# Kernel tuning notes

Measured on AMD Instinct MI355X. Metric: run time of the kernel, lower is better.

## Reference

```python
import jax, jax.numpy as jnp
import numpy as np

N = 8192          # number of prototypes
D = 128           # proto_dim == hidden_dim (residual requires equality)
H = 2             # GAT heads
K = 3             # k_neighbors + 1 (k_neighbors=2 hard-coded in forward)
NEG_SLOPE = 0.2   # PyG GATConv default leaky relu slope
LN_EPS = 1e-5


def setup_inputs() -> dict:
    key = jax.random.key(0)
    ks = jax.random.split(key, 6)
    prototypes = jax.random.normal(ks[0], (N, D), dtype=jnp.float32)
    labels = jax.random.randint(ks[1], (N,), 0, 1024, dtype=jnp.int64)
    # GATConv params: lin maps D -> H*D (concat=False => per-head dim = hidden_dim)
    W = jax.random.normal(ks[2], (D, H * D), dtype=jnp.float32) / np.sqrt(D)
    att_src = jax.random.normal(ks[3], (H, D), dtype=jnp.float32) / np.sqrt(D)
    att_dst = jax.random.normal(ks[4], (H, D), dtype=jnp.float32) / np.sqrt(D)
    bias = jnp.zeros((D,), dtype=jnp.float32)
    gamma = jnp.ones((D,), dtype=jnp.float32)   # LayerNorm weight
    beta = jnp.zeros((D,), dtype=jnp.float32)   # LayerNorm bias
    return {"prototypes": prototypes, "labels": labels, "W": W,
            "att_src": att_src, "att_dst": att_dst, "bias": bias,
            "gamma": gamma, "beta": beta}


def _knn_edges(x):
    # Squared euclidean distances (same ordering as torch.cdist -> same topk indices).
    sq = jnp.sum(x * x, axis=-1)
    d2 = sq[:, None] + sq[None, :] - 2.0 * (x @ x.T)          # [N, N]
    _, idx = jax.lax.top_k(-d2, K)                            # [N, K] smallest dists
    # topk includes self (dist 0); module masks self-edges then GATConv re-adds
    # self loops, so the effective edge set is exactly the topk set -> static E=N*K.
    src = jnp.repeat(jnp.arange(x.shape[0]), K)               # edge source j
    dst = idx.reshape(-1)                                     # edge target i
    return src, dst


def _gat(x, src, dst, W, att_src, att_dst, bias):
    n = x.shape[0]
    xp = (x @ W).reshape(n, H, D)                             # [N, H, C]
    a_s = jnp.sum(xp * att_src[None], axis=-1)                # [N, H]
    a_d = jnp.sum(xp * att_dst[None], axis=-1)                # [N, H]
    e = a_s[src] + a_d[dst]                                   # [E, H]
    e = jax.nn.leaky_relu(e, NEG_SLOPE)
    # segment softmax over incoming edges of each destination node
    m = jax.ops.segment_max(e, dst, num_segments=n)           # [N, H]
    w = jnp.exp(e - m[dst])
    denom = jax.ops.segment_sum(w, dst, num_segments=n)       # [N, H]
    alpha = w / denom[dst]                                    # [E, H]
    msg = alpha[:, :, None] * xp[src]                         # [E, H, C]
    out = jax.ops.segment_sum(msg, dst, num_segments=n)       # [N, H, C]
    return out.mean(axis=1) + bias                            # concat=False -> head mean


def reference(prototypes, labels, W, att_src, att_dst, bias, gamma, beta):
    x = prototypes
    src, dst = _knn_edges(x)
    x_new = _gat(x, src, dst, W, att_src, att_dst, bias)
    mu = jnp.mean(x_new, axis=-1, keepdims=True)
    var = jnp.var(x_new, axis=-1, keepdims=True)
    x_new = (x_new - mu) * jax.lax.rsqrt(var + LN_EPS) * gamma + beta
    x_new = jax.nn.relu(x_new)
    # dropout layers are identity in eval mode
    return x + x_new
```

## Files before the change

### kernel.cpp

```cpp
#include <hip/hip_runtime.h>
#include <hip/hip_bf16.h>
#include <math.h>

#define GN 8192
#define GD 128
#define GH 2
#define GK 3
#define NEG_SLOPE 0.2f
#define LN_EPS 1e-5f

using short8  = __attribute__((ext_vector_type(8)))  short;
using float16 = __attribute__((ext_vector_type(16))) float;
using f32x4   = __attribute__((ext_vector_type(4)))  float;

__device__ __forceinline__ float wred(float v) {
    #pragma unroll
    for (int o = 32; o > 0; o >>= 1) v += __shfl_xor(v, o, 64);
    return v;
}

__device__ __forceinline__ unsigned fenc(float f) {
    unsigned b = __float_as_uint(f);
    return (b & 0x80000000u) ? ~b : (b | 0x80000000u);
}

__device__ __forceinline__ float rawbf2f(unsigned short s) {
    return __uint_as_float(((unsigned)s) << 16);
}
__device__ __forceinline__ unsigned short f2rawbf(float f) {
    __hip_bfloat16 b = __float2bfloat16(f);
    unsigned short r; __builtin_memcpy(&r, &b, 2);
    return r;
}
__device__ __forceinline__ unsigned umin2(unsigned a, unsigned b) { return a < b ? a : b; }
__device__ __forceinline__ unsigned umax2(unsigned a, unsigned b) { return a > b ? a : b; }

__global__ void k_zero(int* p, int n) {
    int t = blockIdx.x * 256 + threadIdx.x;
    if (t < n) p[t] = 0;
}

__global__ void k_uvec(const float* __restrict__ W, const float* __restrict__ att_src,
                       const float* __restrict__ att_dst, float* __restrict__ uvec) {
    __shared__ float vs[128];
    int b = blockIdx.x, t = threadIdx.x;
    int h = b & 1;
    const float* v = (b < 2 ? att_src : att_dst) + h * 128;
    if (t < 128) vs[t] = v[t];
    __syncthreads();
    int d = t >> 1, half = t & 1;
    const float* wr = W + (size_t)d * 256 + h * 128 + half * 64;
    float s = 0.f;
    for (int c = 0; c < 64; c++) s += wr[c] * vs[half * 64 + c];
    s += __shfl_xor(s, 1, 64);
    if (half == 0) uvec[b * 128 + d] = s;
}

__global__ void k_trans(const float* __restrict__ W,
                        unsigned short* __restrict__ Wth, unsigned short* __restrict__ Wtl) {
    int e = blockIdx.x * 256 + threadIdx.x;
    int d = e >> 8, j = e & 255;
    int h = j >> 7, c = j & 127;
    int k = h * 128 + d;
    float w = W[e];
    unsigned short hi = f2rawbf(w);
    Wth[c * 256 + k] = hi;
    Wtl[c * 256 + k] = f2rawbf(w - rawbf2f(hi));
}

__global__ void k_conv(const float* __restrict__ x, const float* __restrict__ uvec,
                       float* __restrict__ sq,
                       unsigned short* __restrict__ xa, unsigned short* __restrict__ xb,
                       float* __restrict__ a_s, float* __restrict__ a_d) {
    int row = blockIdx.x * 4 + (threadIdx.x >> 6);
    int lane = threadIdx.x & 63;
    const float* xr = x + (size_t)row * GD;
    float a0 = xr[lane], a1 = xr[lane + 64];
    float s = wred(a0 * a0 + a1 * a1);
    unsigned short* ar = xa + (size_t)row * 144;
    unsigned short* br = xb + (size_t)row * 144;
    ar[lane] = f2rawbf(-2.f * a0); ar[lane + 64] = f2rawbf(-2.f * a1);
    br[lane] = f2rawbf(a0);        br[lane + 64] = f2rawbf(a1);
    float s0 = wred(a0 * uvec[lane]       + a1 * uvec[64 + lane]);
    float s1 = wred(a0 * uvec[128 + lane] + a1 * uvec[192 + lane]);
    float d0 = wred(a0 * uvec[256 + lane] + a1 * uvec[320 + lane]);
    float d1 = wred(a0 * uvec[384 + lane] + a1 * uvec[448 + lane]);
    if (lane < 16) {
        unsigned short av = 0, bv = 0;
        if (lane == 0)      { av = f2rawbf(s + 512.f); bv = 0x3F80; }
        else if (lane == 1) { float hi = rawbf2f(f2rawbf(s + 512.f));
                              av = f2rawbf(s + 512.f - hi); bv = 0x3F80; }
        ar[128 + lane] = av; br[128 + lane] = bv;
        if (lane == 0) {
            sq[row] = s;
            a_s[row * 2] = s0; a_s[row * 2 + 1] = s1;
            a_d[row * 2] = d0; a_d[row * 2 + 1] = d1;
        }
    }
}

struct Top6 {
    unsigned a0, a1, a2, a3, a4, a5;
    __device__ __forceinline__ void init() { a0=a1=a2=a3=a4=a5=0xFFFFFFFFu; }
    __device__ __forceinline__ void insert(unsigned k) {
        unsigned m0 = umax2(a0, k);  a0 = umin2(a0, k);
        unsigned m1 = umax2(a1, m0); a1 = umin2(a1, m0);
        unsigned m2 = umax2(a2, m1); a2 = umin2(a2, m1);
        unsigned m3 = umax2(a3, m2); a3 = umin2(a3, m2);
        unsigned m4 = umax2(a4, m3); a4 = umin2(a4, m3);
        a5 = umin2(a5, m4);
    }
};

__launch_bounds__(256, 2)
__global__ void k_gemm_topk(const unsigned short* __restrict__ xa,
                            const unsigned short* __restrict__ xb,
                            unsigned* __restrict__ cand) {
    __shared__ unsigned short At[18 * 128 * 8];
    int t = threadIdx.x;
    int w = t >> 6, lane = t & 63, h = lane >> 5, n = lane & 31;
    int col = blockIdx.x * 128 + w * 32 + n;
    int sb = blockIdx.y;

    short8 bfrag[9];
    #pragma unroll
    for (int kc = 0; kc < 9; kc++)
        bfrag[kc] = *(const short8*)(xb + (size_t)col * 144 + (2 * kc + h) * 8);

    Top6 T; T.init();

    for (int it = 0; it < 8; it++) {
        int rowbase = sb * 1024 + it * 128;
        __syncthreads();
        #pragma unroll
        for (int q = t; q < 18 * 128; q += 256) {
            int kb = q >> 7, r = q & 127;
            *(uint4*)&At[(kb * 128 + r) * 8] =
                *(const uint4*)(xa + (size_t)(rowbase + r) * 144 + kb * 8);
        }
        __syncthreads();

        float16 acc[4];
        #pragma unroll
        for (int rs = 0; rs < 4; rs++) acc[rs] = (float16)(0.f);

        #pragma unroll
        for (int kc = 0; kc < 9; kc++) {
            short8 a[4];
            #pragma unroll
            for (int rs = 0; rs < 4; rs++)
                a[rs] = *(const short8*)&At[((2 * kc + h) * 128 + rs * 32 + n) * 8];
            #pragma unroll
            for (int rs = 0; rs < 4; rs++)
                acc[rs] = __builtin_amdgcn_mfma_f32_32x32x16_bf16(a[rs], bfrag[kc], acc[rs], 0, 0, 0);
        }

        #pragma unroll
        for (int rs = 0; rs < 4; rs++) {
            float16 A = acc[rs];
            int rb = rowbase + 4 * h + rs * 32;
            unsigned kk[16];
            #pragma unroll
            for (int r = 0; r < 16; r++)
                kk[r] = (__float_as_uint(A[r]) & 0xFFFFE000u) |
                        (unsigned)(rb + (r & 3) + 8 * (r >> 2));
            unsigned ma = umin2(umin2(umin2(kk[0],kk[1]),umin2(kk[2],kk[3])),
                                umin2(umin2(kk[4],kk[5]),umin2(kk[6],kk[7])));
            unsigned mb = umin2(umin2(umin2(kk[8],kk[9]),umin2(kk[10],kk[11])),
                                umin2(umin2(kk[12],kk[13]),umin2(kk[14],kk[15])));
            if (umin2(ma, mb) <= T.a5) {
                #pragma unroll
                for (int r = 0; r < 16; r++) T.insert(kk[r]);
            }
        }
    }

    unsigned p0 = (unsigned)__shfl_xor((int)T.a0, 32), p1 = (unsigned)__shfl_xor((int)T.a1, 32),
             p2 = (unsigned)__shfl_xor((int)T.a2, 32), p3 = (unsigned)__shfl_xor((int)T.a3, 32),
             p4 = (unsigned)__shfl_xor((int)T.a4, 32), p5 = (unsigned)__shfl_xor((int)T.a5, 32);
    T.insert(p0); T.insert(p1); T.insert(p2); T.insert(p3); T.insert(p4); T.insert(p5);

    if (h == 0) {
        unsigned* c0 = cand + (size_t)col * 48 + sb * 6;
        c0[0]=T.a0; c0[1]=T.a1; c0[2]=T.a2; c0[3]=T.a3; c0[4]=T.a4; c0[5]=T.a5;
    }
}

__device__ __forceinline__ int clampN(int v) {
    return v < 0 ? 0 : (v >= GN ? GN - 1 : v);
}

__global__ void k_refine(const unsigned* __restrict__ cand,
                         const float* __restrict__ x, const float* __restrict__ sq,
                         int* __restrict__ fidx, int* __restrict__ cnt) {
    __shared__ float xjs[4][132];
    int t = threadIdx.x, wv = t >> 6, lane = t & 63;
    int j = blockIdx.x * 4 + wv;
    xjs[wv][lane] = x[(size_t)j * GD + lane];
    xjs[wv][64 + lane] = x[(size_t)j * GD + 64 + lane];
    float sqj = sq[j];
    unsigned long long key = ~0ull;
    if (lane < 48) {
        int idx = (int)(cand[(size_t)j * 48 + lane] & 8191u);
        const float* xi = x + (size_t)idx * GD;
        float p = 0.f;
        #pragma unroll
        for (int d4 = 0; d4 < 32; d4++) {
            float4 a = *(const float4*)(xi + d4 * 4);
            float4 b = *(const float4*)&xjs[wv][d4 * 4];
            p += a.x * b.x + a.y * b.y + a.z * b.z + a.w * b.w;
        }
        float d2 = sqj + sq[idx] - 2.f * p;
        key = ((unsigned long long)fenc(d2) << 32) | (unsigned)idx;
    }
    int out3[3];
    #pragma unroll
    for (int r = 0; r < 3; r++) {
        unsigned long long k = key;
        #pragma unroll
        for (int o = 32; o > 0; o >>= 1) {
            unsigned long long other = __shfl_xor(k, o, 64);
            k = k < other ? k : other;
        }
        out3[r] = (int)(unsigned)(k & 0xffffffffu);
        key = (key == k) ? ~0ull : key;
    }
    if (lane == 0) {
        int i0 = clampN(out3[0]), i1 = clampN(out3[1]), i2 = clampN(out3[2]);
        fidx[j * 3 + 0] = i0; fidx[j * 3 + 1] = i1; fidx[j * 3 + 2] = i2;
        atomicAdd(&cnt[i0], 1); atomicAdd(&cnt[i1], 1); atomicAdd(&cnt[i2], 1);
    }
}

__global__ void k_scan(const int* __restrict__ cnt, int* __restrict__ offs) {
    __shared__ int part[256];
    int t = threadIdx.x;
    int base = t * 32;
    int loc[32];
    int s = 0;
    #pragma unroll
    for (int k = 0; k < 32; k++) { loc[k] = s; s += cnt[base + k]; }
    part[t] = s;
    __syncthreads();
    if (t == 0) {
        int run = 0;
        for (int k = 0; k < 256; k++) { int v = part[k]; part[k] = run; run += v; }
        offs[GN] = run;
    }
    __syncthreads();
    int b = part[t];
    #pragma unroll
    for (int k = 0; k < 32; k++) offs[base + k] = b + loc[k];
}

__global__ void k_fill(const int* __restrict__ fidx, const int* __restrict__ offs,
                       int* __restrict__ cursor, int* __restrict__ elist,
                       const float* __restrict__ a_s, const float* __restrict__ a_d,
                       float2* __restrict__ ew) {
    int eid = blockIdx.x * 256 + threadIdx.x;
    int i = clampN(fidx[eid]);
    int src = eid / 3;
    float2 as = ((const float2*)a_s)[src];
    float2 ad = ((const float2*)a_d)[i];
    float e0 = as.x + ad.x; e0 = e0 >= 0.f ? e0 : NEG_SLOPE * e0;
    float e1 = as.y + ad.y; e1 = e1 >= 0.f ? e1 : NEG_SLOPE * e1;
    float w0 = expf(e0), w1 = expf(e1);
    int pos = atomicAdd(&cursor[i], 1);
    int slot = offs[i] + pos;
    if (slot < GN * GK) { elist[slot] = src; ew[slot] = make_float2(w0, w1); }
}

__launch_bounds__(512, 4)
__global__ void k_out(const int* __restrict__ offs, const int* __restrict__ elst,
                      const float2* __restrict__ ew,
                      const float* __restrict__ x,
                      const unsigned short* __restrict__ Wth,
                      const unsigned short* __restrict__ Wtl,
                      const float* __restrict__ bias, const float* __restrict__ gamma,
                      const float* __restrict__ beta, float* __restrict__ out) {
    __shared__ unsigned short zh[16][264];
    __shared__ unsigned short zl[16][264];
    __shared__ float os[16][132];
    int t = threadIdx.x, i0 = blockIdx.x * 16;
    int wv = t >> 6, lane = t & 63;
    int eslot = lane >> 3, g = lane & 7;

    #pragma unroll
    for (int pp = 0; pp < 2; pp++) {
        int r = wv * 2 + pp, node = i0 + r;
        int s = offs[node], e = offs[node + 1];
        float acc0[16], acc1[16];
        #pragma unroll
        for (int q = 0; q < 16; q++) { acc0[q] = 0.f; acc1[q] = 0.f; }
        float w0s = 0.f, w1s = 0.f;
        for (int k0 = s; k0 < e; k0 += 8) {
            int k = k0 + eslot;
            bool valid = k < e;
            int j = valid ? elst[k] : 0;
            float2 wv2 = valid ? ew[k] : make_float2(0.f, 0.f);
            const float* xr = x + (size_t)j * GD + g * 16;
            float4 x0 = *(const float4*)(xr);
            float4 x1 = *(const float4*)(xr + 4);
            float4 x2 = *(const float4*)(xr + 8);
            float4 x3 = *(const float4*)(xr + 12);
            float xv[16] = {x0.x, x0.y, x0.z, x0.w, x1.x, x1.y, x1.z, x1.w,
                            x2.x, x2.y, x2.z, x2.w, x3.x, x3.y, x3.z, x3.w};
            #pragma unroll
            for (int q = 0; q < 16; q++) {
                acc0[q] += wv2.x * xv[q];
                acc1[q] += wv2.y * xv[q];
            }
            w0s += wv2.x; w1s += wv2.y;
        }
        #pragma unroll
        for (int m = 8; m <= 32; m <<= 1) {
            #pragma unroll
            for (int q = 0; q < 16; q++) {
                acc0[q] += __shfl_xor(acc0[q], m, 64);
                acc1[q] += __shfl_xor(acc1[q], m, 64);
            }
            w0s += __shfl_xor(w0s, m, 64);
            w1s += __shfl_xor(w1s, m, 64);
        }
        if (lane < 8) {
            float dn0 = 0.5f / w0s, dn1 = 0.5f / w1s;
            #pragma unroll
            for (int q = 0; q < 16; q += 2) {
                float a0 = acc0[q] * dn0, a1 = acc0[q + 1] * dn0;
                unsigned short h0 = f2rawbf(a0), h1 = f2rawbf(a1);
                *(unsigned*)&zh[r][lane * 16 + q] = (unsigned)h0 | ((unsigned)h1 << 16);
                *(unsigned*)&zl[r][lane * 16 + q] =
                    (unsigned)f2rawbf(a0 - rawbf2f(h0)) |
                    ((unsigned)f2rawbf(a1 - rawbf2f(h1)) << 16);
                float b0 = acc1[q] * dn1, b1 = acc1[q + 1] * dn1;
                unsigned short p0 = f2rawbf(b0), p1 = f2rawbf(b1);
                *(unsigned*)&zh[r][128 + lane * 16 + q] = (unsigned)p0 | ((unsigned)p1 << 16);
                *(unsigned*)&zl[r][128 + lane * 16 + q] =
                    (unsigned)f2rawbf(b0 - rawbf2f(p0)) |
                    ((unsigned)f2rawbf(b1 - rawbf2f(p1)) << 16);
            }
        }
    }
    __syncthreads();

    {
        int qd = lane >> 4, an = lane & 15;
        int c = wv * 16 + an;
        f32x4 acc = {0.f, 0.f, 0.f, 0.f};
        #pragma unroll
        for (int s = 0; s < 8; s++) {
            int ko = s * 32 + qd * 8;
            short8 ah = *(const short8*)&zh[an][ko];
            short8 al = *(const short8*)&zl[an][ko];
            short8 bh = *(const short8*)(Wth + (size_t)c * 256 + ko);
            short8 bl = *(const short8*)(Wtl + (size_t)c * 256 + ko);
            acc = __builtin_amdgcn_mfma_f32_16x16x32_bf16(ah, bh, acc, 0, 0, 0);
            acc = __builtin_amdgcn_mfma_f32_16x16x32_bf16(al, bh, acc, 0, 0, 0);
            acc = __builtin_amdgcn_mfma_f32_16x16x32_bf16(ah, bl, acc, 0, 0, 0);
        }
        #pragma unroll
        for (int r = 0; r < 4; r++) os[qd * 4 + r][c] = acc[r];
    }
    __syncthreads();

    #pragma unroll
    for (int pp = 0; pp < 2; pp++) {
        int r = wv * 2 + pp, node = i0 + r;
        float y0 = os[r][lane] + bias[lane];
        float y1 = os[r][lane + 64] + bias[lane + 64];
        float mu = wred(y0 + y1) * (1.f / 128.f);
        float c0 = y0 - mu, c1 = y1 - mu;
        float var = wred(c0 * c0 + c1 * c1) * (1.f / 128.f);
        float rs2 = 1.f / sqrtf(var + LN_EPS);
        float n0 = c0 * rs2 * gamma[lane] + beta[lane];
        float n1 = c1 * rs2 * gamma[lane + 64] + beta[lane + 64];
        n0 = n0 > 0.f ? n0 : 0.f;
        n1 = n1 > 0.f ? n1 : 0.f;
        out[(size_t)node * GD + lane]      = x[(size_t)node * GD + lane] + n0;
        out[(size_t)node * GD + lane + 64] = x[(size_t)node * GD + lane + 64] + n1;
    }
}

extern "C" void kernel_launch(void* const* d_in, const int* in_sizes, int n_in,
                              void* d_out, int out_size, void* d_ws, size_t ws_size,
                              hipStream_t stream) {
    const float* x       = (const float*)d_in[0];
    const float* W       = (const float*)d_in[2];
    const float* att_src = (const float*)d_in[3];
    const float* att_dst = (const float*)d_in[4];
    const float* bias    = (const float*)d_in[5];
    const float* gamma   = (const float*)d_in[6];
    const float* beta    = (const float*)d_in[7];
    float* out = (float*)d_out;

    char* w = (char*)d_ws;
    unsigned short* xa = (unsigned short*)w; w += (size_t)GN * 144 * 2;
    unsigned short* xb = (unsigned short*)w; w += (size_t)GN * 144 * 2;
    unsigned* cand = (unsigned*)w;           w += (size_t)GN * 48 * 4;
    float2* ew  = (float2*)w; w += (size_t)GN * GK * 8;
    unsigned short* Wth = (unsigned short*)w; w += (size_t)256 * 128 * 2;
    unsigned short* Wtl = (unsigned short*)w; w += (size_t)256 * 128 * 2;
    float* uvec = (float*)w; w += (size_t)4 * 128 * 4;
    float* sq   = (float*)w; w += (size_t)GN * 4;
    float* a_s  = (float*)w; w += (size_t)GN * GH * 4;
    float* a_d  = (float*)w; w += (size_t)GN * GH * 4;
    int*   fidx = (int*)w;   w += (size_t)GN * GK * 4;
    int*   cnt  = (int*)w;   w += (size_t)GN * 4;
    int*   curs = (int*)w;   w += (size_t)GN * 4;
    int*   offs = (int*)w;   w += (size_t)(GN + 1) * 4;
    int*   elst = (int*)w;   w += (size_t)GN * GK * 4;
    size_t need = (size_t)((char*)w - (char*)d_ws);
    if (ws_size < need) return;

    k_zero<<<(2 * GN + 255) / 256, 256, 0, stream>>>(cnt, 2 * GN);
    k_uvec<<<4, 256, 0, stream>>>(W, att_src, att_dst, uvec);
    k_trans<<<128, 256, 0, stream>>>(W, Wth, Wtl);
    k_conv<<<GN / 4, 256, 0, stream>>>(x, uvec, sq, xa, xb, a_s, a_d);
    k_gemm_topk<<<dim3(64, 8), 256, 0, stream>>>(xa, xb, cand);
    k_refine<<<GN / 4, 256, 0, stream>>>(cand, x, sq, fidx, cnt);
    k_scan<<<1, 256, 0, stream>>>(cnt, offs);
    k_fill<<<GN * GK / 256, 256, 0, stream>>>(fidx, offs, curs, elst, a_s, a_d, ew);
    k_out<<<GN / 16, 512, 0, stream>>>(offs, elst, ew, x, Wth, Wtl, bias, gamma, beta, out);
}
```

Before: 199.4 us.

## Split kNN top-k into more row blocks with top-4 and async LDS loads

Row splits in the GEMM+topk kernel go from 8 to 16, so the grid doubles and each block keeps a top-4 candidate list instead of top-6. This gives 64 candidates per column for the refine step, which now uses all 64 lanes. Tile loads use global_load_lds direct-to-LDS, the launch-bounds occupancy hint rises to 4, and the key masking is deferred until after the early-exit check. The zero, uvec and transpose kernels are merged into k_pre and k_conv to cut launches, at the risk of missing a true neighbour when more than 4 fall in one 512-row split.

```diff
diff --git a/kernel.cpp b/kernel.cpp
--- a/kernel.cpp
+++ b/kernel.cpp
@@ -35,43 +35,41 @@
 __device__ __forceinline__ unsigned umin2(unsigned a, unsigned b) { return a < b ? a : b; }
 __device__ __forceinline__ unsigned umax2(unsigned a, unsigned b) { return a > b ? a : b; }
 
-__global__ void k_zero(int* p, int n) {
-    int t = blockIdx.x * 256 + threadIdx.x;
-    if (t < n) p[t] = 0;
-}
-
-__global__ void k_uvec(const float* __restrict__ W, const float* __restrict__ att_src,
-                       const float* __restrict__ att_dst, float* __restrict__ uvec) {
+__global__ void k_pre(const float* __restrict__ W, const float* __restrict__ att_src,
+                      const float* __restrict__ att_dst,
+                      unsigned short* __restrict__ Wth, unsigned short* __restrict__ Wtl,
+                      float* __restrict__ uvec) {
     __shared__ float vs[128];
     int b = blockIdx.x, t = threadIdx.x;
-    int h = b & 1;
-    const float* v = (b < 2 ? att_src : att_dst) + h * 128;
-    if (t < 128) vs[t] = v[t];
-    __syncthreads();
-    int d = t >> 1, half = t & 1;
-    const float* wr = W + (size_t)d * 256 + h * 128 + half * 64;
-    float s = 0.f;
-    for (int c = 0; c < 64; c++) s += wr[c] * vs[half * 64 + c];
-    s += __shfl_xor(s, 1, 64);
-    if (half == 0) uvec[b * 128 + d] = s;
-}
-
-__global__ void k_trans(const float* __restrict__ W,
-                        unsigned short* __restrict__ Wth, unsigned short* __restrict__ Wtl) {
-    int e = blockIdx.x * 256 + threadIdx.x;
-    int d = e >> 8, j = e & 255;
-    int h = j >> 7, c = j & 127;
-    int k = h * 128 + d;
-    float w = W[e];
-    unsigned short hi = f2rawbf(w);
-    Wth[c * 256 + k] = hi;
-    Wtl[c * 256 + k] = f2rawbf(w - rawbf2f(hi));
+    if (b < 128) {
+        int e = b * 256 + t;
+        int d = e >> 8, j = e & 255;
+        int h = j >> 7, c = j & 127;
+        int k = h * 128 + d;
+        float w = W[e];
+        unsigned short hi = f2rawbf(w);
+        Wth[c * 256 + k] = hi;
+        Wtl[c * 256 + k] = f2rawbf(w - rawbf2f(hi));
+    } else {
+        int bb = b - 128;
+        int h = bb & 1;
+        const float* v = (bb < 2 ? att_src : att_dst) + h * 128;
+        if (t < 128) vs[t] = v[t];
+        __syncthreads();
+        int d = t >> 1, half = t & 1;
+        const float* wr = W + (size_t)d * 256 + h * 128 + half * 64;
+        float s = 0.f;
+        for (int c = 0; c < 64; c++) s += wr[c] * vs[half * 64 + c];
+        s += __shfl_xor(s, 1, 64);
+        if (half == 0) uvec[bb * 128 + d] = s;
+    }
 }
 
 __global__ void k_conv(const float* __restrict__ x, const float* __restrict__ uvec,
                        float* __restrict__ sq,
                        unsigned short* __restrict__ xa, unsigned short* __restrict__ xb,
-                       float* __restrict__ a_s, float* __restrict__ a_d) {
+                       float* __restrict__ a_s, float* __restrict__ a_d,
+                       int* __restrict__ cnt, int* __restrict__ curs) {
     int row = blockIdx.x * 4 + (threadIdx.x >> 6);
     int lane = threadIdx.x & 63;
     const float* xr = x + (size_t)row * GD;
@@ -95,24 +93,12 @@
             sq[row] = s;
             a_s[row * 2] = s0; a_s[row * 2 + 1] = s1;
             a_d[row * 2] = d0; a_d[row * 2 + 1] = d1;
-        }
-    }
-}
-
-struct Top6 {
-    unsigned a0, a1, a2, a3, a4, a5;
-    __device__ __forceinline__ void init() { a0=a1=a2=a3=a4=a5=0xFFFFFFFFu; }
-    __device__ __forceinline__ void insert(unsigned k) {
-        unsigned m0 = umax2(a0, k);  a0 = umin2(a0, k);
-        unsigned m1 = umax2(a1, m0); a1 = umin2(a1, m0);
-        unsigned m2 = umax2(a2, m1); a2 = umin2(a2, m1);
-        unsigned m3 = umax2(a3, m2); a3 = umin2(a3, m2);
-        unsigned m4 = umax2(a4, m3); a4 = umin2(a4, m3);
-        a5 = umin2(a5, m4);
-    }
-};
-
-__launch_bounds__(256, 2)
+            cnt[row] = 0; curs[row] = 0;
+        }
+    }
+}
+
+__launch_bounds__(256, 4)
 __global__ void k_gemm_topk(const unsigned short* __restrict__ xa,
                             const unsigned short* __restrict__ xb,
                             unsigned* __restrict__ cand) {
@@ -127,16 +113,20 @@
     for (int kc = 0; kc < 9; kc++)
         bfrag[kc] = *(const short8*)(xb + (size_t)col * 144 + (2 * kc + h) * 8);
 
-    Top6 T; T.init();
-
-    for (int it = 0; it < 8; it++) {
-        int rowbase = sb * 1024 + it * 128;
+    unsigned T0 = 0xFFFFFFFFu, T1 = 0xFFFFFFFFu, T2 = 0xFFFFFFFFu, T3 = 0xFFFFFFFFu;
+
+    for (int it = 0; it < 4; it++) {
+        int rowbase = sb * 512 + it * 128;
         __syncthreads();
         #pragma unroll
-        for (int q = t; q < 18 * 128; q += 256) {
+        for (int s = 0; s < 9; s++) {
+            int q = t + 256 * s;
             int kb = q >> 7, r = q & 127;
-            *(uint4*)&At[(kb * 128 + r) * 8] =
-                *(const uint4*)(xa + (size_t)(rowbase + r) * 144 + kb * 8);
+            __builtin_amdgcn_global_load_lds(
+                (const __attribute__((address_space(1))) unsigned*)
+                    (xa + (size_t)(rowbase + r) * 144 + kb * 8),
+                (__attribute__((address_space(3))) unsigned*)&At[q * 8],
+                16, 0, 0);
         }
         __syncthreads();
 
@@ -158,31 +148,42 @@
         #pragma unroll
         for (int rs = 0; rs < 4; rs++) {
             float16 A = acc[rs];
-            int rb = rowbase + 4 * h + rs * 32;
-            unsigned kk[16];
-            #pragma unroll
-            for (int r = 0; r < 16; r++)
-                kk[r] = (__float_as_uint(A[r]) & 0xFFFFE000u) |
-                        (unsigned)(rb + (r & 3) + 8 * (r >> 2));
-            unsigned ma = umin2(umin2(umin2(kk[0],kk[1]),umin2(kk[2],kk[3])),
-                                umin2(umin2(kk[4],kk[5]),umin2(kk[6],kk[7])));
-            unsigned mb = umin2(umin2(umin2(kk[8],kk[9]),umin2(kk[10],kk[11])),
-                                umin2(umin2(kk[12],kk[13]),umin2(kk[14],kk[15])));
-            if (umin2(ma, mb) <= T.a5) {
+            unsigned b[16];
+            #pragma unroll
+            for (int r = 0; r < 16; r++) b[r] = __float_as_uint(A[r]);
+            unsigned ma = umin2(umin2(umin2(b[0],b[1]),umin2(b[2],b[3])),
+                                umin2(umin2(b[4],b[5]),umin2(b[6],b[7])));
+            unsigned mb = umin2(umin2(umin2(b[8],b[9]),umin2(b[10],b[11])),
+                                umin2(umin2(b[12],b[13]),umin2(b[14],b[15])));
+            if ((umin2(ma, mb) & 0xFFFFE000u) <= T3) {
+                int rb = rowbase + 4 * h + rs * 32;
                 #pragma unroll
-                for (int r = 0; r < 16; r++) T.insert(kk[r]);
+                for (int r = 0; r < 16; r++) {
+                    unsigned k = (b[r] & 0xFFFFE000u) |
+                                 (unsigned)(rb + (r & 3) + 8 * (r >> 2));
+                    unsigned m0 = umax2(T0, k);  T0 = umin2(T0, k);
+                    unsigned m1 = umax2(T1, m0); T1 = umin2(T1, m0);
+                    unsigned m2 = umax2(T2, m1); T2 = umin2(T2, m1);
+                    T3 = umin2(T3, m2);
+                }
             }
         }
     }
 
-    unsigned p0 = (unsigned)__shfl_xor((int)T.a0, 32), p1 = (unsigned)__shfl_xor((int)T.a1, 32),
-             p2 = (unsigned)__shfl_xor((int)T.a2, 32), p3 = (unsigned)__shfl_xor((int)T.a3, 32),
-             p4 = (unsigned)__shfl_xor((int)T.a4, 32), p5 = (unsigned)__shfl_xor((int)T.a5, 32);
-    T.insert(p0); T.insert(p1); T.insert(p2); T.insert(p3); T.insert(p4); T.insert(p5);
+    unsigned p0 = (unsigned)__shfl_xor((int)T0, 32), p1 = (unsigned)__shfl_xor((int)T1, 32),
+             p2 = (unsigned)__shfl_xor((int)T2, 32), p3 = (unsigned)__shfl_xor((int)T3, 32);
+    #pragma unroll
+    for (int q = 0; q < 4; q++) {
+        unsigned k = (q == 0) ? p0 : (q == 1) ? p1 : (q == 2) ? p2 : p3;
+        unsigned m0 = umax2(T0, k);  T0 = umin2(T0, k);
+        unsigned m1 = umax2(T1, m0); T1 = umin2(T1, m0);
+        unsigned m2 = umax2(T2, m1); T2 = umin2(T2, m1);
+        T3 = umin2(T3, m2);
+    }
 
     if (h == 0) {
-        unsigned* c0 = cand + (size_t)col * 48 + sb * 6;
-        c0[0]=T.a0; c0[1]=T.a1; c0[2]=T.a2; c0[3]=T.a3; c0[4]=T.a4; c0[5]=T.a5;
+        uint4 o = make_uint4(T0, T1, T2, T3);
+        *(uint4*)(cand + (size_t)col * 64 + sb * 4) = o;
     }
 }
 
@@ -199,20 +200,17 @@
     xjs[wv][lane] = x[(size_t)j * GD + lane];
     xjs[wv][64 + lane] = x[(size_t)j * GD + 64 + lane];
     float sqj = sq[j];
-    unsigned long long key = ~0ull;
-    if (lane < 48) {
-        int idx = (int)(cand[(size_t)j * 48 + lane] & 8191u);
-        const float* xi = x + (size_t)idx * GD;
-        float p = 0.f;
-        #pragma unroll
-        for (int d4 = 0; d4 < 32; d4++) {
-            float4 a = *(const float4*)(xi + d4 * 4);
-            float4 b = *(const float4*)&xjs[wv][d4 * 4];
-            p += a.x * b.x + a.y * b.y + a.z * b.z + a.w * b.w;
-        }
-        float d2 = sqj + sq[idx] - 2.f * p;
-        key = ((unsigned long long)fenc(d2) << 32) | (unsigned)idx;
-    }
+    int idx = (int)(cand[(size_t)j * 64 + lane] & 8191u);
+    const float* xi = x + (size_t)idx * GD;
+    float p = 0.f;
+    #pragma unroll
+    for (int d4 = 0; d4 < 32; d4++) {
+        float4 a = *(const float4*)(xi + d4 * 4);
+        float4 b = *(const float4*)&xjs[wv][d4 * 4];
+        p += a.x * b.x + a.y * b.y + a.z * b.z + a.w * b.w;
+    }
+    float d2 = sqj + sq[idx] - 2.f * p;
+    unsigned long long key = ((unsigned long long)fenc(d2) << 32) | (unsigned)idx;
     int out3[3];
     #pragma unroll
     for (int r = 0; r < 3; r++) {
@@ -396,7 +394,7 @@
     char* w = (char*)d_ws;
     unsigned short* xa = (unsigned short*)w; w += (size_t)GN * 144 * 2;
     unsigned short* xb = (unsigned short*)w; w += (size_t)GN * 144 * 2;
-    unsigned* cand = (unsigned*)w;           w += (size_t)GN * 48 * 4;
+    unsigned* cand = (unsigned*)w;           w += (size_t)GN * 64 * 4;
     float2* ew  = (float2*)w; w += (size_t)GN * GK * 8;
     unsigned short* Wth = (unsigned short*)w; w += (size_t)256 * 128 * 2;
     unsigned short* Wtl = (unsigned short*)w; w += (size_t)256 * 128 * 2;
@@ -412,11 +410,9 @@
     size_t need = (size_t)((char*)w - (char*)d_ws);
     if (ws_size < need) return;
 
-    k_zero<<<(2 * GN + 255) / 256, 256, 0, stream>>>(cnt, 2 * GN);
-    k_uvec<<<4, 256, 0, stream>>>(W, att_src, att_dst, uvec);
-    k_trans<<<128, 256, 0, stream>>>(W, Wth, Wtl);
-    k_conv<<<GN / 4, 256, 0, stream>>>(x, uvec, sq, xa, xb, a_s, a_d);
-    k_gemm_topk<<<dim3(64, 8), 256, 0, stream>>>(xa, xb, cand);
+    k_pre<<<132, 256, 0, stream>>>(W, att_src, att_dst, Wth, Wtl, uvec);
+    k_conv<<<GN / 4, 256, 0, stream>>>(x, uvec, sq, xa, xb, a_s, a_d, cnt, curs);
+    k_gemm_topk<<<dim3(64, 16), 256, 0, stream>>>(xa, xb, cand);
     k_refine<<<GN / 4, 256, 0, stream>>>(cand, x, sq, fidx, cnt);
     k_scan<<<1, 256, 0, stream>>>(cnt, offs);
     k_fill<<<GN * GK / 256, 256, 0, stream>>>(fidx, offs, curs, elst, a_s, a_d, ew);
```

New measurement: 192.7 us. -3.3%, faster.
